# Optimization experiments

Measured on AMD Instinct MI355X. Metric: run time of the kernel, lower is better.

Reference implementation:

```python
import jax, jax.numpy as jnp
import numpy as np

B, S, D, H = 2, 4096, 1024, 16
DK = D // H


def setup_inputs() -> dict:
    key = jax.random.key(0)
    ks = jax.random.split(key, 8)
    scale = 1.0 / np.sqrt(D)
    return {
        "q": jax.random.normal(ks[0], (B, S, D), dtype=jnp.float32),
        "k": jax.random.normal(ks[1], (B, S, D), dtype=jnp.float32),
        "v": jax.random.normal(ks[2], (B, S, D), dtype=jnp.float32),
        "mask": jax.random.randint(ks[3], (1, 1, S, S), 0, 2, dtype=jnp.int32),
        "w_q": jax.random.normal(ks[4], (D, D), dtype=jnp.float32) * scale,
        "w_k": jax.random.normal(ks[5], (D, D), dtype=jnp.float32) * scale,
        "w_v": jax.random.normal(ks[6], (D, D), dtype=jnp.float32) * scale,
        "w_o": jax.random.normal(ks[7], (D, D), dtype=jnp.float32) * scale,
    }


def reference(q, k, v, mask, w_q, w_k, w_v, w_o):
    # torch Linear(bias=False): y = x @ W.T
    def proj_split(x, w):
        y = jnp.einsum("bsd,ed->bse", x, w)  # [B,S,D]
        return y.reshape(x.shape[0], -1, H, DK).transpose(0, 2, 1, 3)  # [B,H,S,dk]

    Q = proj_split(q, w_q)
    K = proj_split(k, w_k)
    V = proj_split(v, w_v)

    scores = jnp.einsum("bhqd,bhkd->bhqk", Q, K) / jnp.sqrt(jnp.float32(DK))
    scores = jnp.where(mask == 0, jnp.float32(-1e9), scores)
    attn = jax.nn.softmax(scores, axis=-1)  # dropout p=0 -> identity
    ctx = jnp.einsum("bhqk,bhkd->bhqd", attn, V)  # [B,H,S,dk]
    ctx = ctx.transpose(0, 2, 1, 3).reshape(q.shape[0], -1, D)  # [B,S,D]
    return jnp.einsum("bsd,ed->bse", ctx, w_o)
```

## Files before the change

### kernel.cpp

```cpp
#include <hip/hip_runtime.h>
#include <math.h>
#include <stdint.h>

constexpr int B = 2, S = 4096, D = 1024, H = 16, DK = 64;
constexpr int M_TOT = B * S;

typedef __attribute__((ext_vector_type(8))) short bf16x8;
typedef __attribute__((ext_vector_type(4))) float f32x4;
typedef __attribute__((ext_vector_type(4))) uint32_t u32x4;
typedef unsigned short u16;

__device__ inline u16 f2bf(float f) {
    uint32_t u = __builtin_bit_cast(uint32_t, f);
    u += 0x7fffu + ((u >> 16) & 1u);
    return (u16)(u >> 16);
}

__device__ inline u16 f2bf_hw(float f) {
    __bf16 h = (__bf16)f;
    return __builtin_bit_cast(u16, h);
}

__device__ inline void gl2lds16(const void* g, void* l) {
    __builtin_amdgcn_global_load_lds((const __attribute__((address_space(1))) void*)g,
                                     (__attribute__((address_space(3))) void*)l, 16, 0, 0);
}

__global__ __launch_bounds__(256) void conv_bf16(const float* __restrict__ s0, const float* __restrict__ s1,
                                                 const float* __restrict__ s2, const float* __restrict__ s3,
                                                 u16* __restrict__ d0, u16* __restrict__ d1,
                                                 u16* __restrict__ d2, u16* __restrict__ d3, int n) {
    const float* s; u16* d;
    switch (blockIdx.y) {
        case 0: s = s0; d = d0; break;
        case 1: s = s1; d = d1; break;
        case 2: s = s2; d = d2; break;
        default: s = s3; d = d3; break;
    }
    const int i = (blockIdx.x * 256 + threadIdx.x) * 4;
    if (i < n) {
        float4 v = *(const float4*)(s + i);
        ushort4 o;
        o.x = f2bf(v.x); o.y = f2bf(v.y); o.z = f2bf(v.z); o.w = f2bf(v.w);
        *(ushort4*)(d + i) = o;
    }
}

__global__ __launch_bounds__(256) void mask_pack(const int* __restrict__ m, uint32_t* __restrict__ out) {
    const int i = blockIdx.x * 256 + threadIdx.x;
    const int base = i * 32;
    uint32_t b = 0;
#pragma unroll
    for (int j = 0; j < 32; ++j) b |= (m[base + j] != 0 ? 1u : 0u) << j;
    out[i] = b;
}

template <typename OutT>
__global__ __launch_bounds__(256) void gemm_bt(const u16* __restrict__ X, const u16* __restrict__ Wm,
                                               OutT* __restrict__ Y, int M, int N, int K, float oscale) {
    __shared__ u16 As[2][128 * 64];
    __shared__ u16 Bs[2][128 * 64];
    const int tid = threadIdx.x;
    const int lane = tid & 63;
    const int wave = tid >> 6;
    const int l15 = lane & 15;
    const int quad = lane >> 4;
    const int i0 = blockIdx.x * 128;
    const int j0 = blockIdx.y * 128;
    const int wm = wave & 1, wn = wave >> 1;
    const int lr = lane >> 3;
    const int lc = (lane & 7) * 8;

    f32x4 zero = {0.f, 0.f, 0.f, 0.f};
    f32x4 acc[4][4];
#pragma unroll
    for (int a = 0; a < 4; ++a)
#pragma unroll
        for (int b2 = 0; b2 < 4; ++b2) acc[a][b2] = zero;

    auto STAGE = [&](int buf, int k0) {
#pragma unroll
        for (int c = 0; c < 4; ++c) {
            const int ch = wave * 4 + c;
            const int row = ch * 8 + lr;
            gl2lds16(X + (size_t)(i0 + row) * K + k0 + lc, &As[buf][ch * 512]);
            gl2lds16(Wm + (size_t)(j0 + row) * K + k0 + lc, &Bs[buf][ch * 512]);
        }
    };

    auto COMPUTE = [&](int buf) {
        bf16x8 af[4][2];
#pragma unroll
        for (int mt = 0; mt < 4; ++mt)
#pragma unroll
            for (int ks = 0; ks < 2; ++ks)
                af[mt][ks] = *(const bf16x8*)&As[buf][(wm * 64 + mt * 16 + l15) * 64 + ks * 32 + quad * 8];
#pragma unroll
        for (int nt = 0; nt < 4; ++nt) {
#pragma unroll
            for (int ks = 0; ks < 2; ++ks) {
                bf16x8 bfr = *(const bf16x8*)&Bs[buf][(wn * 64 + nt * 16 + l15) * 64 + ks * 32 + quad * 8];
#pragma unroll
                for (int mt = 0; mt < 4; ++mt)
                    acc[mt][nt] = __builtin_amdgcn_mfma_f32_16x16x32_bf16(af[mt][ks], bfr, acc[mt][nt], 0, 0, 0);
            }
        }
    };

    const int KT = K >> 6;
    STAGE(0, 0);
    asm volatile("s_waitcnt vmcnt(0)" ::: "memory");
    __builtin_amdgcn_s_barrier();
    __builtin_amdgcn_sched_barrier(0);
    for (int t = 0; t < KT; t += 2) {
        if (t + 1 < KT) STAGE(1, (t + 1) << 6);
        COMPUTE(0);
        asm volatile("s_waitcnt vmcnt(0)" ::: "memory");
        __builtin_amdgcn_s_barrier();
        __builtin_amdgcn_sched_barrier(0);
        if (t + 2 < KT) STAGE(0, (t + 2) << 6);
        if (t + 1 < KT) {
            COMPUTE(1);
            asm volatile("s_waitcnt vmcnt(0)" ::: "memory");
            __builtin_amdgcn_s_barrier();
            __builtin_amdgcn_sched_barrier(0);
        }
    }

#pragma unroll
    for (int mt = 0; mt < 4; ++mt) {
#pragma unroll
        for (int r = 0; r < 4; ++r) {
            const int gi = i0 + wm * 64 + mt * 16 + quad * 4 + r;
#pragma unroll
            for (int nt = 0; nt < 4; ++nt) {
                const int gj = j0 + wn * 64 + nt * 16 + l15;
                const float v = acc[mt][nt][r] * oscale;
                if constexpr (sizeof(OutT) == 2) {
                    Y[(size_t)gi * N + gj] = (OutT)f2bf(v);
                } else {
                    Y[(size_t)gi * N + gj] = v;
                }
            }
        }
    }
}

struct KVStage {
    bf16x8 rk[2];
    uint64_t rva[2], rvb[2];
    uint64_t rm[2];
};

__global__ __launch_bounds__(256) void attn_mfma(const u16* __restrict__ Qb, const u16* __restrict__ Kb,
                                                 const u16* __restrict__ Vt,
                                                 const uint64_t* __restrict__ mask64,
                                                 u16* __restrict__ ctx) {
    __shared__ u16 Ks[64 * 64];
    __shared__ u16 Vs[64 * 64];
    const int tid = threadIdx.x;
    const int lane = tid & 63;
    const int wave = tid >> 6;
    const int l15 = lane & 15;
    const int quad = lane >> 4;

    const int bid = blockIdx.y * (S / 128) + blockIdx.x;
    const int xcd = bid & 7;
    const int loc = bid >> 3;
    const int bh = xcd * 4 + (loc >> 5);
    const int q0 = (loc & 31) * 128;

    const int bb = bh >> 4, hh = bh & 15;
    const int mbase = bb * S;
    const int e0 = hh * DK;
    const int swr = ((l15 & 3) << 1) | ((l15 >> 2) & 1);

    const int srow = tid >> 2;
    const int scb = tid & 3;
    const int sws = ((srow & 3) << 1) | ((srow >> 2) & 1);

    bf16x8 aq[2][2];
#pragma unroll
    for (int mi = 0; mi < 2; ++mi) {
        const u16* qrow = Qb + (size_t)(mbase + q0 + wave * 32 + mi * 16 + l15) * D + e0;
        aq[mi][0] = *(const bf16x8*)(qrow + quad * 8);
        aq[mi][1] = *(const bf16x8*)(qrow + 32 + quad * 8);
    }

    f32x4 O[2][4];
    f32x4 Ol[2];
#pragma unroll
    for (int mi = 0; mi < 2; ++mi) {
        Ol[mi] = (f32x4){0.f, 0.f, 0.f, 0.f};
#pragma unroll
        for (int dt = 0; dt < 4; ++dt) O[mi][dt] = (f32x4){0.f, 0.f, 0.f, 0.f};
    }

    bf16x8 ONES;
#pragma unroll
    for (int i = 0; i < 8; ++i) ONES[i] = (short)0x3F80;

    const uint64_t* mrow[2];
#pragma unroll
    for (int mi = 0; mi < 2; ++mi)
        mrow[mi] = mask64 + (size_t)(q0 + wave * 32 + mi * 16 + l15) * (S / 64);

    auto LOADT = [&](KVStage& st, int kt) {
        const int kb = kt * 64;
#pragma unroll
        for (int it = 0; it < 2; ++it) {
            const int cb = scb + it * 4;
            st.rk[it] = *(const bf16x8*)(Kb + (size_t)(mbase + kb + srow) * D + e0 + cb * 8);
            const int k0v = 32 * (cb >> 2) + 4 * (cb & 3);
            const u16* vsrc = Vt + (size_t)(e0 + srow) * M_TOT + mbase + kb + k0v;
            st.rva[it] = *(const uint64_t*)(vsrc);
            st.rvb[it] = *(const uint64_t*)(vsrc + 16);
        }
#pragma unroll
        for (int mi = 0; mi < 2; ++mi) st.rm[mi] = mrow[mi][kt];
    };

    auto WRITET = [&](const KVStage& st) {
#pragma unroll
        for (int it = 0; it < 2; ++it) {
            const int cb = scb + it * 4;
            const int phys = cb ^ sws;
            *(bf16x8*)&Ks[srow * 64 + phys * 8] = st.rk[it];
            const u32x4 vv = {(uint32_t)st.rva[it], (uint32_t)(st.rva[it] >> 32),
                              (uint32_t)st.rvb[it], (uint32_t)(st.rvb[it] >> 32)};
            *(u32x4*)&Vs[srow * 64 + phys * 8] = vv;
        }
    };

    auto COMPUTE = [&](const KVStage& st) {
        bf16x8 kf[4][2];
#pragma unroll
        for (int nt = 0; nt < 4; ++nt) {
            kf[nt][0] = *(const bf16x8*)&Ks[(nt * 16 + l15) * 64 + (quad ^ swr) * 8];
            kf[nt][1] = *(const bf16x8*)&Ks[(nt * 16 + l15) * 64 + ((quad + 4) ^ swr) * 8];
        }

        bf16x8 ap[2][2];
#pragma unroll
        for (int mi = 0; mi < 2; ++mi) {
            f32x4 sa[4];
            __builtin_amdgcn_s_setprio(1);
#pragma unroll
            for (int nt = 0; nt < 4; ++nt) {
                f32x4 c = {0.f, 0.f, 0.f, 0.f};
                c = __builtin_amdgcn_mfma_f32_16x16x32_bf16(kf[nt][0], aq[mi][0], c, 0, 0, 0);
                c = __builtin_amdgcn_mfma_f32_16x16x32_bf16(kf[nt][1], aq[mi][1], c, 0, 0, 0);
                sa[nt] = c;
            }
            __builtin_amdgcn_s_setprio(0);
            const uint64_t mw = st.rm[mi];
            const uint32_t mlo = (uint32_t)(mw >> (quad * 4));
            const uint32_t mhi = (uint32_t)(mw >> (quad * 4 + 32));
            uint32_t pk[4][2];
#pragma unroll
            for (int nt = 0; nt < 4; ++nt) {
                const uint32_t mx = (nt < 2) ? mlo : mhi;
                float p[4];
#pragma unroll
                for (int r = 0; r < 4; ++r) {
                    const float e = __builtin_amdgcn_exp2f(sa[nt][r]);
                    p[r] = ((mx >> ((nt & 1) * 16 + r)) & 1u) ? e : 0.f;
                }
                pk[nt][0] = (uint32_t)f2bf_hw(p[0]) | ((uint32_t)f2bf_hw(p[1]) << 16);
                pk[nt][1] = (uint32_t)f2bf_hw(p[2]) | ((uint32_t)f2bf_hw(p[3]) << 16);
            }
            const u32x4 w0 = {pk[0][0], pk[0][1], pk[1][0], pk[1][1]};
            const u32x4 w1 = {pk[2][0], pk[2][1], pk[3][0], pk[3][1]};
            ap[mi][0] = __builtin_bit_cast(bf16x8, w0);
            ap[mi][1] = __builtin_bit_cast(bf16x8, w1);
        }

        __builtin_amdgcn_s_setprio(1);
#pragma unroll
        for (int mi = 0; mi < 2; ++mi) {
            Ol[mi] = __builtin_amdgcn_mfma_f32_16x16x32_bf16(ap[mi][0], ONES, Ol[mi], 0, 0, 0);
            Ol[mi] = __builtin_amdgcn_mfma_f32_16x16x32_bf16(ap[mi][1], ONES, Ol[mi], 0, 0, 0);
        }
#pragma unroll
        for (int dt = 0; dt < 4; ++dt) {
            const bf16x8 bv0 = *(const bf16x8*)&Vs[(dt * 16 + l15) * 64 + (quad ^ swr) * 8];
            const bf16x8 bv1 = *(const bf16x8*)&Vs[(dt * 16 + l15) * 64 + ((quad + 4) ^ swr) * 8];
#pragma unroll
            for (int mi = 0; mi < 2; ++mi) {
                O[mi][dt] = __builtin_amdgcn_mfma_f32_16x16x32_bf16(ap[mi][0], bv0, O[mi][dt], 0, 0, 0);
                O[mi][dt] = __builtin_amdgcn_mfma_f32_16x16x32_bf16(ap[mi][1], bv1, O[mi][dt], 0, 0, 0);
            }
        }
        __builtin_amdgcn_s_setprio(0);
    };

    KVStage stA, stB;
    LOADT(stA, 0);
    for (int kt = 0; kt < S / 64; kt += 2) {
        LOADT(stB, kt + 1);
        __builtin_amdgcn_s_barrier();
        WRITET(stA);
        asm volatile("s_waitcnt lgkmcnt(0)" ::: "memory");
        __builtin_amdgcn_s_barrier();
        __builtin_amdgcn_sched_barrier(0);
        COMPUTE(stA);

        if (kt + 2 < S / 64) LOADT(stA, kt + 2);
        __builtin_amdgcn_s_barrier();
        WRITET(stB);
        asm volatile("s_waitcnt lgkmcnt(0)" ::: "memory");
        __builtin_amdgcn_s_barrier();
        __builtin_amdgcn_sched_barrier(0);
        COMPUTE(stB);
    }

#pragma unroll
    for (int mi = 0; mi < 2; ++mi) {
#pragma unroll
        for (int r = 0; r < 4; ++r) {
            const float inv = 1.f / Ol[mi][r];
            const int gm = mbase + q0 + wave * 32 + mi * 16 + quad * 4 + r;
#pragma unroll
            for (int dt = 0; dt < 4; ++dt)
                ctx[(size_t)gm * D + e0 + dt * 16 + l15] = f2bf(O[mi][dt][r] * inv);
        }
    }
}

extern "C" void kernel_launch(void* const* d_in, const int* in_sizes, int n_in,
                              void* d_out, int out_size, void* d_ws, size_t ws_size,
                              hipStream_t stream) {
    (void)in_sizes; (void)n_in; (void)out_size; (void)ws_size;
    const float* q = (const float*)d_in[0];
    const float* k = (const float*)d_in[1];
    const float* v = (const float*)d_in[2];
    const int* msk = (const int*)d_in[3];
    const float* w_q = (const float*)d_in[4];
    const float* w_k = (const float*)d_in[5];
    const float* w_v = (const float*)d_in[6];
    const float* w_o = (const float*)d_in[7];
    float* out = (float*)d_out;

    const size_t MB = 1u << 20;
    char* w = (char*)d_ws;
    u16* qb   = (u16*)(w + 0 * MB);
    u16* kb   = (u16*)(w + 16 * MB);
    u16* vb   = (u16*)(w + 32 * MB);
    u16* wqb  = (u16*)(w + 48 * MB);
    u16* wkb  = (u16*)(w + 50 * MB);
    u16* wvb  = (u16*)(w + 52 * MB);
    u16* wob  = (u16*)(w + 54 * MB);
    uint64_t* maskb = (uint64_t*)(w + 56 * MB);
    u16* Qf   = (u16*)(w + 58 * MB);
    u16* Kf   = (u16*)(w + 74 * MB);
    u16* Vtf  = (u16*)(w + 90 * MB);
    u16* ctxb = (u16*)(w + 106 * MB);

    const float SCL2 = 0.18033688011112042f;

    dim3 blk(256);
    conv_bf16<<<dim3(8192, 3), blk, 0, stream>>>(q, k, v, q, qb, kb, vb, qb, M_TOT * D);
    conv_bf16<<<dim3(1024, 4), blk, 0, stream>>>(w_q, w_k, w_v, w_o, wqb, wkb, wvb, wob, D * D);
    mask_pack<<<dim3(S * S / 32 / 256), blk, 0, stream>>>(msk, (uint32_t*)maskb);

    gemm_bt<u16><<<dim3(M_TOT / 128, D / 128), blk, 0, stream>>>(qb, wqb, Qf, M_TOT, D, D, SCL2);
    gemm_bt<u16><<<dim3(M_TOT / 128, D / 128), blk, 0, stream>>>(kb, wkb, Kf, M_TOT, D, D, 1.0f);
    gemm_bt<u16><<<dim3(D / 128, M_TOT / 128), blk, 0, stream>>>(wvb, vb, Vtf, D, M_TOT, D, 1.0f);

    attn_mfma<<<dim3(S / 128, B * H), blk, 0, stream>>>(Qf, Kf, Vtf, maskb, ctxb);

    gemm_bt<float><<<dim3(M_TOT / 128, D / 128), blk, 0, stream>>>(ctxb, wob, out, M_TOT, D, D, 1.0f);
}
```

Before: 518.1 us.

## Load K fragments directly from global, double-buffer V in LDS with single barrier

K tiles now go straight from global memory into MFMA register fragments, prefetched one tile ahead, so the K staging through LDS and its reads are gone. V is double-buffered in shared memory with a simpler XOR swizzle, and each tile step uses one barrier instead of two, with the next tile's V written during softmax. This is meant to cut LDS traffic and synchronisation stalls, at the cost of more live registers and less coalesced per-lane K global loads.

```diff
diff --git a/kernel.cpp b/kernel.cpp
--- a/kernel.cpp
+++ b/kernel.cpp
@@ -147,7 +147,6 @@
 }
 
 struct KVStage {
-    bf16x8 rk[2];
     uint64_t rva[2], rvb[2];
     uint64_t rm[2];
 };
@@ -156,8 +155,7 @@
                                                  const u16* __restrict__ Vt,
                                                  const uint64_t* __restrict__ mask64,
                                                  u16* __restrict__ ctx) {
-    __shared__ u16 Ks[64 * 64];
-    __shared__ u16 Vs[64 * 64];
+    __shared__ u16 Vs[2][64 * 64];
     const int tid = threadIdx.x;
     const int lane = tid & 63;
     const int wave = tid >> 6;
@@ -173,11 +171,10 @@
     const int bb = bh >> 4, hh = bh & 15;
     const int mbase = bb * S;
     const int e0 = hh * DK;
-    const int swr = ((l15 & 3) << 1) | ((l15 >> 2) & 1);
+    const int r7 = l15 & 7;
 
     const int srow = tid >> 2;
     const int scb = tid & 3;
-    const int sws = ((srow & 3) << 1) | ((srow >> 2) & 1);
 
     bf16x8 aq[2][2];
 #pragma unroll
@@ -205,12 +202,22 @@
     for (int mi = 0; mi < 2; ++mi)
         mrow[mi] = mask64 + (size_t)(q0 + wave * 32 + mi * 16 + l15) * (S / 64);
 
-    auto LOADT = [&](KVStage& st, int kt) {
+    bf16x8 kf[4][2];
+    auto KFLOAD = [&](int kt) {
+        const int kb = kt * 64;
+#pragma unroll
+        for (int nt = 0; nt < 4; ++nt) {
+            const u16* krow = Kb + (size_t)(mbase + kb + nt * 16 + l15) * D + e0;
+            kf[nt][0] = *(const bf16x8*)(krow + quad * 8);
+            kf[nt][1] = *(const bf16x8*)(krow + 32 + quad * 8);
+        }
+    };
+
+    auto LOADV = [&](KVStage& st, int kt) {
         const int kb = kt * 64;
 #pragma unroll
         for (int it = 0; it < 2; ++it) {
             const int cb = scb + it * 4;
-            st.rk[it] = *(const bf16x8*)(Kb + (size_t)(mbase + kb + srow) * D + e0 + cb * 8);
             const int k0v = 32 * (cb >> 2) + 4 * (cb & 3);
             const u16* vsrc = Vt + (size_t)(e0 + srow) * M_TOT + mbase + kb + k0v;
             st.rva[it] = *(const uint64_t*)(vsrc);
@@ -220,40 +227,38 @@
         for (int mi = 0; mi < 2; ++mi) st.rm[mi] = mrow[mi][kt];
     };
 
-    auto WRITET = [&](const KVStage& st) {
+    auto WRITEV = [&](const KVStage& st, int buf) {
 #pragma unroll
         for (int it = 0; it < 2; ++it) {
             const int cb = scb + it * 4;
-            const int phys = cb ^ sws;
-            *(bf16x8*)&Ks[srow * 64 + phys * 8] = st.rk[it];
-            const u32x4 vv = {(uint32_t)st.rva[it], (uint32_t)(st.rva[it] >> 32),
-                              (uint32_t)st.rvb[it], (uint32_t)(st.rvb[it] >> 32)};
-            *(u32x4*)&Vs[srow * 64 + phys * 8] = vv;
-        }
-    };
-
-    auto COMPUTE = [&](const KVStage& st) {
-        bf16x8 kf[4][2];
-#pragma unroll
-        for (int nt = 0; nt < 4; ++nt) {
-            kf[nt][0] = *(const bf16x8*)&Ks[(nt * 16 + l15) * 64 + (quad ^ swr) * 8];
-            kf[nt][1] = *(const bf16x8*)&Ks[(nt * 16 + l15) * 64 + ((quad + 4) ^ swr) * 8];
-        }
-
-        bf16x8 ap[2][2];
-#pragma unroll
-        for (int mi = 0; mi < 2; ++mi) {
-            f32x4 sa[4];
-            __builtin_amdgcn_s_setprio(1);
+            const int phys = cb ^ (srow & 7);
+            *(uint64_t*)&Vs[buf][srow * 64 + phys * 8] = st.rva[it];
+            *(uint64_t*)&Vs[buf][srow * 64 + phys * 8 + 4] = st.rvb[it];
+        }
+    };
+
+    constexpr int NT = S / 64;
+
+    auto DO_HALF = [&](int kt, int buf, KVStage& stW, KVStage& stX) {
+        f32x4 sa[2][4];
+        __builtin_amdgcn_s_setprio(1);
+#pragma unroll
+        for (int mi = 0; mi < 2; ++mi)
 #pragma unroll
             for (int nt = 0; nt < 4; ++nt) {
                 f32x4 c = {0.f, 0.f, 0.f, 0.f};
                 c = __builtin_amdgcn_mfma_f32_16x16x32_bf16(kf[nt][0], aq[mi][0], c, 0, 0, 0);
                 c = __builtin_amdgcn_mfma_f32_16x16x32_bf16(kf[nt][1], aq[mi][1], c, 0, 0, 0);
-                sa[nt] = c;
-            }
-            __builtin_amdgcn_s_setprio(0);
-            const uint64_t mw = st.rm[mi];
+                sa[mi][nt] = c;
+            }
+        __builtin_amdgcn_s_setprio(0);
+
+        if (kt + 1 < NT) KFLOAD(kt + 1);
+
+        bf16x8 ap[2][2];
+#pragma unroll
+        for (int mi = 0; mi < 2; ++mi) {
+            const uint64_t mw = stX.rm[mi];
             const uint32_t mlo = (uint32_t)(mw >> (quad * 4));
             const uint32_t mhi = (uint32_t)(mw >> (quad * 4 + 32));
             uint32_t pk[4][2];
@@ -263,7 +268,7 @@
                 float p[4];
 #pragma unroll
                 for (int r = 0; r < 4; ++r) {
-                    const float e = __builtin_amdgcn_exp2f(sa[nt][r]);
+                    const float e = __builtin_amdgcn_exp2f(sa[mi][nt][r]);
                     p[r] = ((mx >> ((nt & 1) * 16 + r)) & 1u) ? e : 0.f;
                 }
                 pk[nt][0] = (uint32_t)f2bf_hw(p[0]) | ((uint32_t)f2bf_hw(p[1]) << 16);
@@ -275,6 +280,8 @@
             ap[mi][1] = __builtin_bit_cast(bf16x8, w1);
         }
 
+        if (kt + 1 < NT) WRITEV(stW, buf ^ 1);
+
         __builtin_amdgcn_s_setprio(1);
 #pragma unroll
         for (int mi = 0; mi < 2; ++mi) {
@@ -283,8 +290,8 @@
         }
 #pragma unroll
         for (int dt = 0; dt < 4; ++dt) {
-            const bf16x8 bv0 = *(const bf16x8*)&Vs[(dt * 16 + l15) * 64 + (quad ^ swr) * 8];
-            const bf16x8 bv1 = *(const bf16x8*)&Vs[(dt * 16 + l15) * 64 + ((quad + 4) ^ swr) * 8];
+            const bf16x8 bv0 = *(const bf16x8*)&Vs[buf][(dt * 16 + l15) * 64 + (quad ^ r7) * 8];
+            const bf16x8 bv1 = *(const bf16x8*)&Vs[buf][(dt * 16 + l15) * 64 + ((quad + 4) ^ r7) * 8];
 #pragma unroll
             for (int mi = 0; mi < 2; ++mi) {
                 O[mi][dt] = __builtin_amdgcn_mfma_f32_16x16x32_bf16(ap[mi][0], bv0, O[mi][dt], 0, 0, 0);
@@ -292,26 +299,26 @@
             }
         }
         __builtin_amdgcn_s_setprio(0);
-    };
-
-    KVStage stA, stB;
-    LOADT(stA, 0);
-    for (int kt = 0; kt < S / 64; kt += 2) {
-        LOADT(stB, kt + 1);
-        __builtin_amdgcn_s_barrier();
-        WRITET(stA);
+
+        if (kt + 2 < NT) LOADV(stX, kt + 2);
+
         asm volatile("s_waitcnt lgkmcnt(0)" ::: "memory");
         __builtin_amdgcn_s_barrier();
         __builtin_amdgcn_sched_barrier(0);
-        COMPUTE(stA);
-
-        if (kt + 2 < S / 64) LOADT(stA, kt + 2);
-        __builtin_amdgcn_s_barrier();
-        WRITET(stB);
-        asm volatile("s_waitcnt lgkmcnt(0)" ::: "memory");
-        __builtin_amdgcn_s_barrier();
-        __builtin_amdgcn_sched_barrier(0);
-        COMPUTE(stB);
+    };
+
+    KVStage stA, stB;
+    LOADV(stA, 0);
+    KFLOAD(0);
+    LOADV(stB, 1);
+    WRITEV(stA, 0);
+    asm volatile("s_waitcnt lgkmcnt(0)" ::: "memory");
+    __builtin_amdgcn_s_barrier();
+    __builtin_amdgcn_sched_barrier(0);
+
+    for (int kt = 0; kt < NT; kt += 2) {
+        DO_HALF(kt, 0, stB, stA);
+        DO_HALF(kt + 1, 1, stA, stB);
     }
 
 #pragma unroll
```

Result: slower. 630.1 us (+21.6%).

## Double-buffer attention K/V LDS tiles and merge QKV projections into one launch

Applied to the files above, without the earlier changes.

The attention kernel now keeps two LDS buffers for the K/V tiles, so the next tile is written while the current one is computed, and each step needs one barrier instead of two. The LDS swizzle becomes a plain row&7 XOR, and V is written as two 64-bit stores. The three Q/K/V projection GEMMs are folded into one launch with a z-dimension switch, which cuts launch overhead and lets the three GEMMs' blocks fill the GPU together. The cost is double the attention LDS footprint, which may lower occupancy, plus extra register pressure from the restructured pipeline.

```diff
diff --git a/kernel.cpp b/kernel.cpp
--- a/kernel.cpp
+++ b/kernel.cpp
@@ -56,17 +56,14 @@
 }
 
 template <typename OutT>
-__global__ __launch_bounds__(256) void gemm_bt(const u16* __restrict__ X, const u16* __restrict__ Wm,
-                                               OutT* __restrict__ Y, int M, int N, int K, float oscale) {
-    __shared__ u16 As[2][128 * 64];
-    __shared__ u16 Bs[2][128 * 64];
+__device__ __forceinline__ void gemm_core(const u16* __restrict__ X, const u16* __restrict__ Wm,
+                                          OutT* __restrict__ Y, int i0, int j0, int N, int K,
+                                          float oscale, u16* As, u16* Bs) {
     const int tid = threadIdx.x;
     const int lane = tid & 63;
     const int wave = tid >> 6;
     const int l15 = lane & 15;
     const int quad = lane >> 4;
-    const int i0 = blockIdx.x * 128;
-    const int j0 = blockIdx.y * 128;
     const int wm = wave & 1, wn = wave >> 1;
     const int lr = lane >> 3;
     const int lc = (lane & 7) * 8;
@@ -83,8 +80,8 @@
         for (int c = 0; c < 4; ++c) {
             const int ch = wave * 4 + c;
             const int row = ch * 8 + lr;
-            gl2lds16(X + (size_t)(i0 + row) * K + k0 + lc, &As[buf][ch * 512]);
-            gl2lds16(Wm + (size_t)(j0 + row) * K + k0 + lc, &Bs[buf][ch * 512]);
+            gl2lds16(X + (size_t)(i0 + row) * K + k0 + lc, &As[buf * 8192 + ch * 512]);
+            gl2lds16(Wm + (size_t)(j0 + row) * K + k0 + lc, &Bs[buf * 8192 + ch * 512]);
         }
     };
 
@@ -94,12 +91,12 @@
         for (int mt = 0; mt < 4; ++mt)
 #pragma unroll
             for (int ks = 0; ks < 2; ++ks)
-                af[mt][ks] = *(const bf16x8*)&As[buf][(wm * 64 + mt * 16 + l15) * 64 + ks * 32 + quad * 8];
+                af[mt][ks] = *(const bf16x8*)&As[buf * 8192 + (wm * 64 + mt * 16 + l15) * 64 + ks * 32 + quad * 8];
 #pragma unroll
         for (int nt = 0; nt < 4; ++nt) {
 #pragma unroll
             for (int ks = 0; ks < 2; ++ks) {
-                bf16x8 bfr = *(const bf16x8*)&Bs[buf][(wn * 64 + nt * 16 + l15) * 64 + ks * 32 + quad * 8];
+                bf16x8 bfr = *(const bf16x8*)&Bs[buf * 8192 + (wn * 64 + nt * 16 + l15) * 64 + ks * 32 + quad * 8];
 #pragma unroll
                 for (int mt = 0; mt < 4; ++mt)
                     acc[mt][nt] = __builtin_amdgcn_mfma_f32_16x16x32_bf16(af[mt][ks], bfr, acc[mt][nt], 0, 0, 0);
@@ -146,6 +143,35 @@
     }
 }
 
+template <typename OutT>
+__global__ __launch_bounds__(256) void gemm_bt(const u16* __restrict__ X, const u16* __restrict__ Wm,
+                                               OutT* __restrict__ Y, int N, int K, float oscale) {
+    __shared__ u16 As[2 * 128 * 64];
+    __shared__ u16 Bs[2 * 128 * 64];
+    gemm_core<OutT>(X, Wm, Y, blockIdx.x * 128, blockIdx.y * 128, N, K, oscale, As, Bs);
+}
+
+__global__ __launch_bounds__(256) void gemm_qkv(const u16* __restrict__ qb, const u16* __restrict__ wqb,
+                                                u16* __restrict__ Qf,
+                                                const u16* __restrict__ kb, const u16* __restrict__ wkb,
+                                                u16* __restrict__ Kf,
+                                                const u16* __restrict__ wvb, const u16* __restrict__ vb,
+                                                u16* __restrict__ Vtf, float scl2) {
+    __shared__ u16 As[2 * 128 * 64];
+    __shared__ u16 Bs[2 * 128 * 64];
+    switch (blockIdx.z) {
+        case 0:
+            gemm_core<u16>(qb, wqb, Qf, blockIdx.x * 128, blockIdx.y * 128, D, D, scl2, As, Bs);
+            break;
+        case 1:
+            gemm_core<u16>(kb, wkb, Kf, blockIdx.x * 128, blockIdx.y * 128, D, D, 1.0f, As, Bs);
+            break;
+        default:
+            gemm_core<u16>(wvb, vb, Vtf, blockIdx.y * 128, blockIdx.x * 128, M_TOT, D, 1.0f, As, Bs);
+            break;
+    }
+}
+
 struct KVStage {
     bf16x8 rk[2];
     uint64_t rva[2], rvb[2];
@@ -156,8 +182,8 @@
                                                  const u16* __restrict__ Vt,
                                                  const uint64_t* __restrict__ mask64,
                                                  u16* __restrict__ ctx) {
-    __shared__ u16 Ks[64 * 64];
-    __shared__ u16 Vs[64 * 64];
+    __shared__ u16 Ks[2][64 * 64];
+    __shared__ u16 Vs[2][64 * 64];
     const int tid = threadIdx.x;
     const int lane = tid & 63;
     const int wave = tid >> 6;
@@ -173,11 +199,10 @@
     const int bb = bh >> 4, hh = bh & 15;
     const int mbase = bb * S;
     const int e0 = hh * DK;
-    const int swr = ((l15 & 3) << 1) | ((l15 >> 2) & 1);
+    const int r7 = l15 & 7;
 
     const int srow = tid >> 2;
     const int scb = tid & 3;
-    const int sws = ((srow & 3) << 1) | ((srow >> 2) & 1);
 
     bf16x8 aq[2][2];
 #pragma unroll
@@ -220,24 +245,23 @@
         for (int mi = 0; mi < 2; ++mi) st.rm[mi] = mrow[mi][kt];
     };
 
-    auto WRITET = [&](const KVStage& st) {
+    auto WRITET = [&](const KVStage& st, int buf) {
 #pragma unroll
         for (int it = 0; it < 2; ++it) {
             const int cb = scb + it * 4;
-            const int phys = cb ^ sws;
-            *(bf16x8*)&Ks[srow * 64 + phys * 8] = st.rk[it];
-            const u32x4 vv = {(uint32_t)st.rva[it], (uint32_t)(st.rva[it] >> 32),
-                              (uint32_t)st.rvb[it], (uint32_t)(st.rvb[it] >> 32)};
-            *(u32x4*)&Vs[srow * 64 + phys * 8] = vv;
+            const int phys = cb ^ (srow & 7);
+            *(bf16x8*)&Ks[buf][srow * 64 + phys * 8] = st.rk[it];
+            *(uint64_t*)&Vs[buf][srow * 64 + phys * 8] = st.rva[it];
+            *(uint64_t*)&Vs[buf][srow * 64 + phys * 8 + 4] = st.rvb[it];
         }
     };
 
-    auto COMPUTE = [&](const KVStage& st) {
+    auto COMPUTE = [&](int buf, const KVStage& st) {
         bf16x8 kf[4][2];
 #pragma unroll
         for (int nt = 0; nt < 4; ++nt) {
-            kf[nt][0] = *(const bf16x8*)&Ks[(nt * 16 + l15) * 64 + (quad ^ swr) * 8];
-            kf[nt][1] = *(const bf16x8*)&Ks[(nt * 16 + l15) * 64 + ((quad + 4) ^ swr) * 8];
+            kf[nt][0] = *(const bf16x8*)&Ks[buf][(nt * 16 + l15) * 64 + (quad ^ r7) * 8];
+            kf[nt][1] = *(const bf16x8*)&Ks[buf][(nt * 16 + l15) * 64 + ((quad + 4) ^ r7) * 8];
         }
 
         bf16x8 ap[2][2];
@@ -283,8 +307,8 @@
         }
 #pragma unroll
         for (int dt = 0; dt < 4; ++dt) {
-            const bf16x8 bv0 = *(const bf16x8*)&Vs[(dt * 16 + l15) * 64 + (quad ^ swr) * 8];
-            const bf16x8 bv1 = *(const bf16x8*)&Vs[(dt * 16 + l15) * 64 + ((quad + 4) ^ swr) * 8];
+            const bf16x8 bv0 = *(const bf16x8*)&Vs[buf][(dt * 16 + l15) * 64 + (quad ^ r7) * 8];
+            const bf16x8 bv1 = *(const bf16x8*)&Vs[buf][(dt * 16 + l15) * 64 + ((quad + 4) ^ r7) * 8];
 #pragma unroll
             for (int mi = 0; mi < 2; ++mi) {
                 O[mi][dt] = __builtin_amdgcn_mfma_f32_16x16x32_bf16(ap[mi][0], bv0, O[mi][dt], 0, 0, 0);
@@ -294,24 +318,30 @@
         __builtin_amdgcn_s_setprio(0);
     };
 
+    constexpr int NT = S / 64;
+
     KVStage stA, stB;
     LOADT(stA, 0);
-    for (int kt = 0; kt < S / 64; kt += 2) {
-        LOADT(stB, kt + 1);
-        __builtin_amdgcn_s_barrier();
-        WRITET(stA);
+    WRITET(stA, 0);
+    LOADT(stB, 1);
+    asm volatile("s_waitcnt lgkmcnt(0)" ::: "memory");
+    __builtin_amdgcn_s_barrier();
+    __builtin_amdgcn_sched_barrier(0);
+
+    for (int kt = 0; kt < NT; kt += 2) {
+        WRITET(stB, 1);
+        COMPUTE(0, stA);
+        if (kt + 2 < NT) LOADT(stA, kt + 2);
         asm volatile("s_waitcnt lgkmcnt(0)" ::: "memory");
         __builtin_amdgcn_s_barrier();
         __builtin_amdgcn_sched_barrier(0);
-        COMPUTE(stA);
-
-        if (kt + 2 < S / 64) LOADT(stA, kt + 2);
-        __builtin_amdgcn_s_barrier();
-        WRITET(stB);
+
+        if (kt + 2 < NT) WRITET(stA, 0);
+        COMPUTE(1, stB);
+        if (kt + 3 < NT) LOADT(stB, kt + 3);
         asm volatile("s_waitcnt lgkmcnt(0)" ::: "memory");
         __builtin_amdgcn_s_barrier();
         __builtin_amdgcn_sched_barrier(0);
-        COMPUTE(stB);
     }
 
 #pragma unroll
@@ -363,11 +393,9 @@
     conv_bf16<<<dim3(1024, 4), blk, 0, stream>>>(w_q, w_k, w_v, w_o, wqb, wkb, wvb, wob, D * D);
     mask_pack<<<dim3(S * S / 32 / 256), blk, 0, stream>>>(msk, (uint32_t*)maskb);
 
-    gemm_bt<u16><<<dim3(M_TOT / 128, D / 128), blk, 0, stream>>>(qb, wqb, Qf, M_TOT, D, D, SCL2);
-    gemm_bt<u16><<<dim3(M_TOT / 128, D / 128), blk, 0, stream>>>(kb, wkb, Kf, M_TOT, D, D, 1.0f);
-    gemm_bt<u16><<<dim3(D / 128, M_TOT / 128), blk, 0, stream>>>(wvb, vb, Vtf, D, M_TOT, D, 1.0f);
+    gemm_qkv<<<dim3(M_TOT / 128, D / 128, 3), blk, 0, stream>>>(qb, wqb, Qf, kb, wkb, Kf, wvb, vb, Vtf, SCL2);
 
     attn_mfma<<<dim3(S / 128, B * H), blk, 0, stream>>>(Qf, Kf, Vtf, maskb, ctxb);
 
-    gemm_bt<float><<<dim3(M_TOT / 128, D / 128), blk, 0, stream>>>(ctxb, wob, out, M_TOT, D, D, 1.0f);
-}
+    gemm_bt<float><<<dim3(M_TOT / 128, D / 128), blk, 0, stream>>>(ctxb, wob, out, D, D, 1.0f);
+}
```

Result: faster. 494.8 us (-4.5%).
